# Kernel optimization log

Hardware: AMD Instinct MI355X
Metric: run time of the kernel (lower is better)

## Reference

```python
import jax, jax.numpy as jnp
import numpy as np

INPUT_SIZE = 512
HIDDEN_SIZE = 512
SEQ_LEN = 1024
BATCH = 64


def setup_inputs() -> dict:
    key = jax.random.key(0)
    ks = jax.random.split(key, 5)
    I, H = INPUT_SIZE, HIDDEN_SIZE
    s_i = 1.0 / np.sqrt(I)
    s_h = 1.0 / np.sqrt(H)
    x = jax.random.normal(ks[0], (SEQ_LEN, BATCH, I), dtype=jnp.float32)
    h0 = jnp.zeros((1, BATCH, H), dtype=jnp.float32)
    c0 = jnp.zeros((1, BATCH, H), dtype=jnp.float32)
    # nn.Linear params: y = x @ W.T + b, uniform(-1/sqrt(fan_in), 1/sqrt(fan_in))
    Wi = jax.random.uniform(ks[1], (4 * H, I), minval=-s_i, maxval=s_i, dtype=jnp.float32)
    bi = jax.random.uniform(ks[2], (4 * H,), minval=-s_i, maxval=s_i, dtype=jnp.float32)
    Wh = jax.random.uniform(ks[3], (4 * H, H), minval=-s_h, maxval=s_h, dtype=jnp.float32)
    bh = jax.random.uniform(ks[4], (4 * H,), minval=-s_h, maxval=s_h, dtype=jnp.float32)
    return {"x": x, "h0": h0, "c0": c0, "Wi": Wi, "bi": bi, "Wh": Wh, "bh": bh}


def reference(x, h0, c0, Wi, bi, Wh, bh):
    # Precompute input contribution for all timesteps: (S, B, 4H)
    x_scores = jnp.einsum('sbi,gi->sbg', x, Wi) + bi

    def step(carry, xg):
        h, c = carry
        gates = xg + h @ Wh.T + bh  # (B, 4H)
        # chunk order in the source: forget, in, cell, out
        f, i, g, o = jnp.split(gates, 4, axis=-1)
        f = jax.nn.sigmoid(f)
        i = jax.nn.sigmoid(i)
        g = jnp.tanh(g)
        o = jax.nn.sigmoid(o)
        c = f * c + i * g
        h = o * jnp.tanh(c)
        return (h, c), h

    (h, c), h_seq = jax.lax.scan(step, (h0[0], c0[0]), x_scores)
    return h_seq, h, c
```

## Files before the change

### kernel.cpp

```cpp
#include <hip/hip_runtime.h>

typedef _Float16 half_t;
typedef _Float16 half8 __attribute__((ext_vector_type(8)));
typedef _Float16 half4_t __attribute__((ext_vector_type(4)));
typedef float v4f __attribute__((ext_vector_type(4)));
typedef unsigned int u32x4 __attribute__((ext_vector_type(4)));

#define SEQ 1024
#define NBATCH 64
#define HDIM 512
#define CREW 32
#define XTILE (NBATCH * HDIM)
#define HSEQ_ELEMS ((size_t)SEQ * NBATCH * HDIM)

__device__ __forceinline__ float fsig(float x)  { return 1.f / (1.f + __expf(-x)); }
__device__ __forceinline__ float ftanh(float x) { return 1.f - 2.f / (__expf(2.f * x) + 1.f); }

__global__ void conv_f2h(const float4* __restrict__ src, half4_t* __restrict__ dst, int n4) {
    int idx = blockIdx.x * blockDim.x + threadIdx.x;
    int stride = gridDim.x * blockDim.x;
    for (int i = idx; i < n4; i += stride) {
        float4 v = src[i];
        half4_t h;
        h[0] = (half_t)v.x; h[1] = (half_t)v.y; h[2] = (half_t)v.z; h[3] = (half_t)v.w;
        dst[i] = h;
    }
}

__global__ void prep_kernel(const float* __restrict__ h0, half_t* __restrict__ hbuf,
                            unsigned int* __restrict__ flags, unsigned int* __restrict__ xtick) {
    int idx = blockIdx.x * 256 + threadIdx.x;
    if (idx < 8) xtick[idx] = 0u;
    if (idx < SEQ * CREW) flags[idx] = 0u;
    if (idx < XTILE) hbuf[idx] = (half_t)h0[idx];
}

__global__ __launch_bounds__(256, 1) void lstm_rec(
    const half_t* __restrict__ xh,
    const half_t* __restrict__ wi,
    const half_t* __restrict__ wh,
    const float*  __restrict__ bi,
    const float*  __restrict__ bh,
    const float*  __restrict__ c0,
    float*        __restrict__ out,
    half_t*       __restrict__ hbuf,
    unsigned int* __restrict__ flags,
    unsigned int* __restrict__ xtick)
{
    unsigned int xcd;
    asm volatile("s_getreg_b32 %0, hwreg(HW_REG_XCC_ID)" : "=s"(xcd));
    xcd &= 7u;
    if (xcd != 0u) return;

    __shared__ unsigned int rank_s;
    if (threadIdx.x == 0) rank_s = atomicAdd(&xtick[0], 1u);
    __syncthreads();
    const unsigned int rank = rank_s;
    if (rank >= CREW) return;

    const int tid    = threadIdx.x;
    const int lane   = tid & 63;
    const int w      = tid >> 6;
    const int lane16 = lane & 15;
    const int lgrp   = lane >> 4;
    const int k8     = lgrp * 8;
    const int j0     = (int)rank * 16;
    const int g      = w * 512 + j0 + lane16;

    half8 bfi[16], bfh[16];
#pragma unroll
    for (int kt = 0; kt < 16; ++kt) {
        bfi[kt] = *(const half8*)&wi[(size_t)g * 512 + kt * 32 + k8];
        bfh[kt] = *(const half8*)&wh[(size_t)g * 512 + kt * 32 + k8];
    }
    const float bsum = bi[g] + bh[g];

    const int mE = w * 16 + lgrp * 4;
    float c[4];
#pragma unroll
    for (int r = 0; r < 4; ++r)
        c[r] = c0[(mE + r) * HDIM + j0 + lane16];

    __shared__ char   hlds[NBATCH * HDIM * 2];
    __shared__ char   xlds[NBATCH * HDIM * 2];
    __shared__ float  glds[4 * 64 * 17];
    __shared__ half_t hsl[NBATCH * 16];

    v4f xa[4];
#pragma unroll
    for (int fm = 0; fm < 4; ++fm) xa[fm] = (v4f)0.f;
#pragma unroll
    for (int kt = 0; kt < 16; ++kt)
#pragma unroll
        for (int fm = 0; fm < 4; ++fm) {
            half8 a = *(const half8*)&xh[(fm * 16 + lane16) * HDIM + kt * 32 + k8];
            xa[fm] = __builtin_amdgcn_mfma_f32_16x16x32_f16(a, bfi[kt], xa[fm], 0, 0, 0);
        }
    __syncthreads();

    for (int t = 0; t < SEQ; ++t) {
        const half_t* hin  = hbuf + (t & 1) * XTILE;
        half_t*       hout = hbuf + ((t + 1) & 1) * XTILE;

        if (t > 0) {
            if (w == 0) {
                const unsigned int* fp = flags + (size_t)(t - 1) * CREW + (lane & 31);
                unsigned int f;
                do {
                    asm volatile("global_load_dword %0, %1, off sc0\n\t"
                                 "s_waitcnt vmcnt(0)"
                                 : "=v"(f) : "v"(fp) : "memory");
                } while (__ballot(f == 0u) != 0ull);
            }
            __syncthreads();
        }

        u32x4 th[16], tx[16];
        {
            const u32x4* hsrc = (const u32x4*)hin;
#pragma unroll
            for (int i = 0; i < 16; ++i)
                asm volatile("global_load_dwordx4 %0, %1, off sc0"
                             : "=v"(th[i]) : "v"(hsrc + i * 256 + tid) : "memory");
            const int tn = (t + 1 < SEQ) ? (t + 1) : t;
            const u32x4* xsrc = (const u32x4*)(xh + (size_t)tn * XTILE);
#pragma unroll
            for (int i = 0; i < 16; ++i)
                asm volatile("global_load_dwordx4 %0, %1, off"
                             : "=v"(tx[i]) : "v"(xsrc + i * 256 + tid) : "memory");
        }

        asm volatile("s_waitcnt vmcnt(16)" ::: "memory");
#pragma unroll
        for (int i = 0; i < 16; ++i) {
            int n    = i * 256 + tid;
            int row  = n >> 6;
            int gran = ((n & 63) + row) & 63;
            *(u32x4*)(hlds + row * 1024 + gran * 16) = th[i];
        }
        asm volatile("s_waitcnt vmcnt(0)" ::: "memory");
#pragma unroll
        for (int i = 0; i < 16; ++i) {
            int n    = i * 256 + tid;
            int row  = n >> 6;
            int gran = ((n & 63) + row) & 63;
            *(u32x4*)(xlds + row * 1024 + gran * 16) = tx[i];
        }
        __syncthreads();

        v4f acc[4];
#pragma unroll
        for (int fm = 0; fm < 4; ++fm) acc[fm] = xa[fm];
#pragma unroll
        for (int kt = 0; kt < 16; ++kt) {
#pragma unroll
            for (int fm = 0; fm < 4; ++fm) {
                const int row  = fm * 16 + lane16;
                const int gran = (kt * 4 + lgrp + row) & 63;
                half8 a = *(const half8*)(hlds + row * 1024 + gran * 16);
                acc[fm] = __builtin_amdgcn_mfma_f32_16x16x32_f16(a, bfh[kt], acc[fm], 0, 0, 0);
            }
        }

#pragma unroll
        for (int fm = 0; fm < 4; ++fm)
#pragma unroll
            for (int r = 0; r < 4; ++r)
                glds[(w * 64 + fm * 16 + lgrp * 4 + r) * 17 + lane16] = acc[fm][r] + bsum;
        __syncthreads();

        const int jcol = j0 + lane16;
        float hv[4];
#pragma unroll
        for (int r = 0; r < 4; ++r) {
            const int m = mE + r;
            float F  = glds[(0 * 64 + m) * 17 + lane16];
            float I  = glds[(1 * 64 + m) * 17 + lane16];
            float G  = glds[(2 * 64 + m) * 17 + lane16];
            float O  = glds[(3 * 64 + m) * 17 + lane16];
            float f  = fsig(F);
            float i  = fsig(I);
            float gg = ftanh(G);
            float o  = fsig(O);
            float cn = f * c[r] + i * gg;
            c[r] = cn;
            hv[r] = o * ftanh(cn);
            hsl[m * 16 + lane16] = (half_t)hv[r];
        }
        __syncthreads();

        if (tid < 128) {
            const int m = tid >> 1;
            half_t* dst = hout + m * HDIM + j0 + (tid & 1) * 8;
            u32x4 val = *(const u32x4*)&hsl[m * 16 + (tid & 1) * 8];
            asm volatile("global_store_dwordx4 %0, %1, off sc0"
                         :: "v"(dst), "v"(val) : "memory");
        }
        asm volatile("s_waitcnt vmcnt(0)" ::: "memory");
        __syncthreads();
        if (tid == 0) {
            unsigned int one = 1u;
            unsigned int* fp = flags + (size_t)t * CREW + rank;
            asm volatile("global_store_dword %0, %1, off sc0"
                         :: "v"(fp), "v"(one) : "memory");
        }

#pragma unroll
        for (int r = 0; r < 4; ++r) {
            const int m = mE + r;
            out[((size_t)t * NBATCH + m) * HDIM + jcol] = hv[r];
            if (t == SEQ - 1) {
                out[HSEQ_ELEMS + (size_t)m * HDIM + jcol] = hv[r];
                out[HSEQ_ELEMS + (size_t)NBATCH * HDIM + (size_t)m * HDIM + jcol] = c[r];
            }
        }

        v4f xn[4];
#pragma unroll
        for (int fm = 0; fm < 4; ++fm) xn[fm] = (v4f)0.f;
#pragma unroll
        for (int kt = 0; kt < 16; ++kt) {
#pragma unroll
            for (int fm = 0; fm < 4; ++fm) {
                const int row  = fm * 16 + lane16;
                const int gran = (kt * 4 + lgrp + row) & 63;
                half8 a = *(const half8*)(xlds + row * 1024 + gran * 16);
                xn[fm] = __builtin_amdgcn_mfma_f32_16x16x32_f16(a, bfi[kt], xn[fm], 0, 0, 0);
            }
        }
#pragma unroll
        for (int fm = 0; fm < 4; ++fm) xa[fm] = xn[fm];
    }
}

extern "C" void kernel_launch(void* const* d_in, const int* in_sizes, int n_in,
                              void* d_out, int out_size, void* d_ws, size_t ws_size,
                              hipStream_t stream) {
    const float* x  = (const float*)d_in[0];
    const float* h0 = (const float*)d_in[1];
    const float* c0 = (const float*)d_in[2];
    const float* Wi = (const float*)d_in[3];
    const float* bi = (const float*)d_in[4];
    const float* Wh = (const float*)d_in[5];
    const float* bh = (const float*)d_in[6];
    float* out = (float*)d_out;

    char* ws = (char*)d_ws;
    unsigned int* xtick = (unsigned int*)(ws + 0);
    unsigned int* flags = (unsigned int*)(ws + 4096);
    half_t*       hbuf  = (half_t*)(ws + 135168);
    half_t*       wi_h  = (half_t*)(ws + 266240);
    half_t*       wh_h  = (half_t*)(ws + 2363392);
    half_t*       x_h   = (half_t*)(ws + 4460544);

    conv_f2h<<<4096, 256, 0, stream>>>((const float4*)x,  (half4_t*)x_h,  (SEQ * NBATCH * HDIM) / 4);
    conv_f2h<<<1024, 256, 0, stream>>>((const float4*)Wi, (half4_t*)wi_h, (4 * HDIM * HDIM) / 4);
    conv_f2h<<<1024, 256, 0, stream>>>((const float4*)Wh, (half4_t*)wh_h, (4 * HDIM * HDIM) / 4);
    prep_kernel<<<128, 256, 0, stream>>>(h0, hbuf, flags, xtick);
    lstm_rec<<<1024, 256, 0, stream>>>(x_h, wi_h, wh_h, bi, bh, c0, out, hbuf, flags, xtick);
}
```

Baseline: 7.757 ms.

## Defer x-tile LDS staging off critical path and vectorize h/c writeback

```diff
diff --git a/kernel.cpp b/kernel.cpp
--- a/kernel.cpp
+++ b/kernel.cpp
@@ -2,9 +2,11 @@
 
 typedef _Float16 half_t;
 typedef _Float16 half8 __attribute__((ext_vector_type(8)));
+typedef _Float16 half4v __attribute__((ext_vector_type(4)));
 typedef _Float16 half4_t __attribute__((ext_vector_type(4)));
 typedef float v4f __attribute__((ext_vector_type(4)));
 typedef unsigned int u32x4 __attribute__((ext_vector_type(4)));
+typedef unsigned int u32x2 __attribute__((ext_vector_type(2)));
 
 #define SEQ 1024
 #define NBATCH 64
@@ -49,14 +51,17 @@
 {
     unsigned int xcd;
     asm volatile("s_getreg_b32 %0, hwreg(HW_REG_XCC_ID)" : "=s"(xcd));
-    xcd &= 7u;
-    if (xcd != 0u) return;
+    if ((xcd & 7u) != 0u) return;
 
     __shared__ unsigned int rank_s;
     if (threadIdx.x == 0) rank_s = atomicAdd(&xtick[0], 1u);
     __syncthreads();
     const unsigned int rank = rank_s;
     if (rank >= CREW) return;
+
+    __shared__ char  hlds[XTILE * 2];
+    __shared__ char  xlds[XTILE * 2];
+    __shared__ float glds[4 * 64 * 17];
 
     const int tid    = threadIdx.x;
     const int lane   = tid & 63;
@@ -75,16 +80,13 @@
     }
     const float bsum = bi[g] + bh[g];
 
-    const int mE = w * 16 + lgrp * 4;
+    const int mrow = w * 16 + (lane >> 2);
+    const int jsub = (lane & 3) * 4;
     float c[4];
-#pragma unroll
-    for (int r = 0; r < 4; ++r)
-        c[r] = c0[(mE + r) * HDIM + j0 + lane16];
-
-    __shared__ char   hlds[NBATCH * HDIM * 2];
-    __shared__ char   xlds[NBATCH * HDIM * 2];
-    __shared__ float  glds[4 * 64 * 17];
-    __shared__ half_t hsl[NBATCH * 16];
+    {
+        float4 cv = *(const float4*)&c0[(size_t)mrow * HDIM + j0 + jsub];
+        c[0] = cv.x; c[1] = cv.y; c[2] = cv.z; c[3] = cv.w;
+    }
 
     v4f xa[4];
 #pragma unroll
@@ -93,10 +95,9 @@
     for (int kt = 0; kt < 16; ++kt)
 #pragma unroll
         for (int fm = 0; fm < 4; ++fm) {
-            half8 a = *(const half8*)&xh[(fm * 16 + lane16) * HDIM + kt * 32 + k8];
+            half8 a = *(const half8*)&xh[(size_t)(fm * 16 + lane16) * HDIM + kt * 32 + k8];
             xa[fm] = __builtin_amdgcn_mfma_f32_16x16x32_f16(a, bfi[kt], xa[fm], 0, 0, 0);
         }
-    __syncthreads();
 
     for (int t = 0; t < SEQ; ++t) {
         const half_t* hin  = hbuf + (t & 1) * XTILE;
@@ -106,11 +107,12 @@
             if (w == 0) {
                 const unsigned int* fp = flags + (size_t)(t - 1) * CREW + (lane & 31);
                 unsigned int f;
+                int guard = 0;
                 do {
                     asm volatile("global_load_dword %0, %1, off sc0\n\t"
                                  "s_waitcnt vmcnt(0)"
-                                 : "=v"(f) : "v"(fp) : "memory");
-                } while (__ballot(f == 0u) != 0ull);
+                                 : "=&v"(f) : "v"(fp) : "memory");
+                } while (__ballot(f == 0u) != 0ull && ++guard < (1 << 18));
             }
             __syncthreads();
         }
@@ -121,30 +123,21 @@
 #pragma unroll
             for (int i = 0; i < 16; ++i)
                 asm volatile("global_load_dwordx4 %0, %1, off sc0"
-                             : "=v"(th[i]) : "v"(hsrc + i * 256 + tid) : "memory");
+                             : "=&v"(th[i]) : "v"(hsrc + i * 256 + tid) : "memory");
             const int tn = (t + 1 < SEQ) ? (t + 1) : t;
             const u32x4* xsrc = (const u32x4*)(xh + (size_t)tn * XTILE);
 #pragma unroll
             for (int i = 0; i < 16; ++i)
                 asm volatile("global_load_dwordx4 %0, %1, off"
-                             : "=v"(tx[i]) : "v"(xsrc + i * 256 + tid) : "memory");
-        }
-
+                             : "=&v"(tx[i]) : "v"(xsrc + i * 256 + tid) : "memory");
+        }
         asm volatile("s_waitcnt vmcnt(16)" ::: "memory");
 #pragma unroll
         for (int i = 0; i < 16; ++i) {
-            int n    = i * 256 + tid;
-            int row  = n >> 6;
-            int gran = ((n & 63) + row) & 63;
-            *(u32x4*)(hlds + row * 1024 + gran * 16) = th[i];
-        }
-        asm volatile("s_waitcnt vmcnt(0)" ::: "memory");
-#pragma unroll
-        for (int i = 0; i < 16; ++i) {
-            int n    = i * 256 + tid;
-            int row  = n >> 6;
-            int gran = ((n & 63) + row) & 63;
-            *(u32x4*)(xlds + row * 1024 + gran * 16) = tx[i];
+            int n   = i * 256 + tid;
+            int row = n >> 6;
+            int gr  = ((n & 63) + row) & 63;
+            *(u32x4*)(hlds + row * 1024 + gr * 16) = th[i];
         }
         __syncthreads();
 
@@ -155,9 +148,9 @@
         for (int kt = 0; kt < 16; ++kt) {
 #pragma unroll
             for (int fm = 0; fm < 4; ++fm) {
-                const int row  = fm * 16 + lane16;
-                const int gran = (kt * 4 + lgrp + row) & 63;
-                half8 a = *(const half8*)(hlds + row * 1024 + gran * 16);
+                const int row = fm * 16 + lane16;
+                const int gr  = (kt * 4 + lgrp + row) & 63;
+                half8 a = *(const half8*)(hlds + row * 1024 + gr * 16);
                 acc[fm] = __builtin_amdgcn_mfma_f32_16x16x32_f16(a, bfh[kt], acc[fm], 0, 0, 0);
             }
         }
@@ -169,32 +162,29 @@
                 glds[(w * 64 + fm * 16 + lgrp * 4 + r) * 17 + lane16] = acc[fm][r] + bsum;
         __syncthreads();
 
-        const int jcol = j0 + lane16;
         float hv[4];
 #pragma unroll
         for (int r = 0; r < 4; ++r) {
-            const int m = mE + r;
-            float F  = glds[(0 * 64 + m) * 17 + lane16];
-            float I  = glds[(1 * 64 + m) * 17 + lane16];
-            float G  = glds[(2 * 64 + m) * 17 + lane16];
-            float O  = glds[(3 * 64 + m) * 17 + lane16];
+            float F  = glds[(0 * 64 + mrow) * 17 + jsub + r];
+            float I  = glds[(1 * 64 + mrow) * 17 + jsub + r];
+            float G  = glds[(2 * 64 + mrow) * 17 + jsub + r];
+            float O  = glds[(3 * 64 + mrow) * 17 + jsub + r];
             float f  = fsig(F);
-            float i  = fsig(I);
+            float i_ = fsig(I);
             float gg = ftanh(G);
             float o  = fsig(O);
-            float cn = f * c[r] + i * gg;
+            float cn = f * c[r] + i_ * gg;
             c[r] = cn;
             hv[r] = o * ftanh(cn);
-            hsl[m * 16 + lane16] = (half_t)hv[r];
-        }
-        __syncthreads();
-
-        if (tid < 128) {
-            const int m = tid >> 1;
-            half_t* dst = hout + m * HDIM + j0 + (tid & 1) * 8;
-            u32x4 val = *(const u32x4*)&hsl[m * 16 + (tid & 1) * 8];
-            asm volatile("global_store_dwordx4 %0, %1, off sc0"
-                         :: "v"(dst), "v"(val) : "memory");
+        }
+
+        {
+            half4v hp;
+#pragma unroll
+            for (int r = 0; r < 4; ++r) hp[r] = (half_t)hv[r];
+            half_t* dst = hout + (size_t)mrow * HDIM + j0 + jsub;
+            asm volatile("global_store_dwordx2 %0, %1, off sc0"
+                         :: "v"(dst), "v"(*(u32x2*)&hp) : "memory");
         }
         asm volatile("s_waitcnt vmcnt(0)" ::: "memory");
         __syncthreads();
@@ -205,31 +195,43 @@
                          :: "v"(fp), "v"(one) : "memory");
         }
 
-#pragma unroll
-        for (int r = 0; r < 4; ++r) {
-            const int m = mE + r;
-            out[((size_t)t * NBATCH + m) * HDIM + jcol] = hv[r];
+        {
+            float4 o4; o4.x = hv[0]; o4.y = hv[1]; o4.z = hv[2]; o4.w = hv[3];
+            *(float4*)&out[((size_t)t * NBATCH + mrow) * HDIM + j0 + jsub] = o4;
             if (t == SEQ - 1) {
-                out[HSEQ_ELEMS + (size_t)m * HDIM + jcol] = hv[r];
-                out[HSEQ_ELEMS + (size_t)NBATCH * HDIM + (size_t)m * HDIM + jcol] = c[r];
-            }
-        }
-
-        v4f xn[4];
-#pragma unroll
-        for (int fm = 0; fm < 4; ++fm) xn[fm] = (v4f)0.f;
-#pragma unroll
-        for (int kt = 0; kt < 16; ++kt) {
-#pragma unroll
-            for (int fm = 0; fm < 4; ++fm) {
-                const int row  = fm * 16 + lane16;
-                const int gran = (kt * 4 + lgrp + row) & 63;
-                half8 a = *(const half8*)(xlds + row * 1024 + gran * 16);
-                xn[fm] = __builtin_amdgcn_mfma_f32_16x16x32_f16(a, bfi[kt], xn[fm], 0, 0, 0);
-            }
-        }
-#pragma unroll
-        for (int fm = 0; fm < 4; ++fm) xa[fm] = xn[fm];
+                *(float4*)&out[HSEQ_ELEMS + (size_t)mrow * HDIM + j0 + jsub] = o4;
+                float4 c4; c4.x = c[0]; c4.y = c[1]; c4.z = c[2]; c4.w = c[3];
+                *(float4*)&out[HSEQ_ELEMS + (size_t)NBATCH * HDIM
+                               + (size_t)mrow * HDIM + j0 + jsub] = c4;
+            }
+        }
+
+#pragma unroll
+        for (int i = 0; i < 16; ++i) {
+            int n   = i * 256 + tid;
+            int row = n >> 6;
+            int gr  = ((n & 63) + row) & 63;
+            *(u32x4*)(xlds + row * 1024 + gr * 16) = tx[i];
+        }
+        __syncthreads();
+
+        if (t + 1 < SEQ) {
+            v4f xn[4];
+#pragma unroll
+            for (int fm = 0; fm < 4; ++fm) xn[fm] = (v4f)0.f;
+#pragma unroll
+            for (int kt = 0; kt < 16; ++kt) {
+#pragma unroll
+                for (int fm = 0; fm < 4; ++fm) {
+                    const int row = fm * 16 + lane16;
+                    const int gr  = (kt * 4 + lgrp + row) & 63;
+                    half8 a = *(const half8*)(xlds + row * 1024 + gr * 16);
+                    xn[fm] = __builtin_amdgcn_mfma_f32_16x16x32_f16(a, bfi[kt], xn[fm], 0, 0, 0);
+                }
+            }
+#pragma unroll
+            for (int fm = 0; fm < 4; ++fm) xa[fm] = xn[fm];
+        }
     }
 }
 
```

Measured after the change: 7.486 ms, median of 4. -3.5%, faster.
